# Kernel optimization log

Hardware: AMD Instinct MI355X
Metric: run time of the kernel (lower is better)

The kernel has to match this reference:

```python
import jax, jax.numpy as jnp
import numpy as np

TEMPERATURE = 0.07
EPS = 1e-8  # torch cosine_similarity norm clamp


def setup_inputs() -> dict:
    key = jax.random.key(0)
    k1, k2 = jax.random.split(key)
    B, d = 8192, 256
    X = jax.random.normal(k1, (B, d), dtype=jnp.float32)
    Y = jax.random.normal(k2, (B, d), dtype=jnp.float32)
    return {"X": X, "Y": Y}


def _normalize(v):
    # torch cosine_similarity clamps the norm at eps
    n = jnp.sqrt(jnp.sum(v * v, axis=-1, keepdims=True))
    return v / jnp.maximum(n, EPS)


def reference(X, Y):
    # cosine similarity matrix via normalize + GEMM (same math as broadcasted
    # cosine_similarity(X.unsqueeze(1), Y.unsqueeze(0), dim=-1))
    Xn = _normalize(X)                      # [B, d]
    Yn = _normalize(Y)                      # [B, d]
    logits = (Xn @ Yn.T) / TEMPERATURE      # [B, B]
    # cross_entropy with targets = arange(B): mean of -log_softmax diagonal
    logp = jax.nn.log_softmax(logits, axis=-1)
    loss = -jnp.mean(jnp.diagonal(logp))
    return loss
```

## Files before the change

kernel.cpp:

```cpp
#include <hip/hip_runtime.h>
#include <hip/hip_bf16.h>


typedef __attribute__((ext_vector_type(2)))  float f32x2;
typedef __attribute__((ext_vector_type(4)))  float f32x4;
typedef __attribute__((ext_vector_type(4)))  int   i32x4;
typedef __attribute__((ext_vector_type(8)))  int   i32x8;

#define AS1(p) ((const __attribute__((address_space(1))) void*)(uintptr_t)(p))
#define AS3(p) ((__attribute__((address_space(3))) void*)(uintptr_t)(p))

constexpr int   BROWS = 8192;
constexpr int   DDIM  = 256;
constexpr float kInvT = 14.285714285714286f;
constexpr float kC1   = 20.609929155556622f;
constexpr float kLn2  = 0.6931471805599453f;
constexpr int   kSC   = 0x7F7F7F7F;

#if __has_builtin(__builtin_amdgcn_exp2f)
#define EXP2F(x) __builtin_amdgcn_exp2f(x)
#else
#define EXP2F(x) exp2f(x)
#endif
#if __has_builtin(__builtin_amdgcn_logf)
#define LOG2F(x) __builtin_amdgcn_logf(x)
#else
#define LOG2F(x) log2f(x)
#endif

static __device__ __forceinline__ unsigned f2fp8(float f) {
  unsigned u = __builtin_bit_cast(unsigned, f);
  unsigned s = (u >> 24) & 0x80u;
  float af = __builtin_fabsf(f);
  if (af < 0.015625f) {
    int q = (int)__builtin_rintf(af * 512.0f);
    return s | (unsigned)q;
  }
  unsigned au = u & 0x7FFFFFFFu;
  au += 0x7FFFFu + ((au >> 20) & 1u);
  unsigned e8 = ((au >> 23) - 127u + 7u) & 0xFu;
  unsigned m  = (au >> 20) & 7u;
  return s | (e8 << 3) | m;
}

__global__ __launch_bounds__(256) void nrm_kernel(
    const float* __restrict__ X, const float* __restrict__ Y,
    unsigned int* __restrict__ Xq, unsigned int* __restrict__ Yq,
    float* __restrict__ diag, float* __restrict__ row_sum)
{
  const int wave = threadIdx.x >> 6;
  const int lane = threadIdx.x & 63;
  const int row  = blockIdx.x * 4 + wave;
  const float4 x = *(const float4*)(X + (size_t)row * DDIM + lane * 4);
  const float4 y = *(const float4*)(Y + (size_t)row * DDIM + lane * 4);
  float ssx = x.x*x.x + x.y*x.y + x.z*x.z + x.w*x.w;
  float ssy = y.x*y.x + y.y*y.y + y.z*y.z + y.w*y.w;
  float dot = x.x*y.x + x.y*y.y + x.z*y.z + x.w*y.w;
  #pragma unroll
  for (int m = 1; m < 64; m <<= 1) {
    ssx += __shfl_xor(ssx, m);
    ssy += __shfl_xor(ssy, m);
    dot += __shfl_xor(dot, m);
  }
  const float invx = 1.0f / fmaxf(sqrtf(ssx), 1e-8f);
  const float invy = 1.0f / fmaxf(sqrtf(ssy), 1e-8f);
#if __has_builtin(__builtin_amdgcn_cvt_pk_fp8_f32)
  int xq = __builtin_amdgcn_cvt_pk_fp8_f32(x.x * invx, x.y * invx, 0, false);
  xq     = __builtin_amdgcn_cvt_pk_fp8_f32(x.z * invx, x.w * invx, xq, true);
  int yq = __builtin_amdgcn_cvt_pk_fp8_f32(y.x * invy, y.y * invy, 0, false);
  yq     = __builtin_amdgcn_cvt_pk_fp8_f32(y.z * invy, y.w * invy, yq, true);
#else
  int xq = (int)(f2fp8(x.x*invx) | (f2fp8(x.y*invx) << 8) |
                 (f2fp8(x.z*invx) << 16) | (f2fp8(x.w*invx) << 24));
  int yq = (int)(f2fp8(y.x*invy) | (f2fp8(y.y*invy) << 8) |
                 (f2fp8(y.z*invy) << 16) | (f2fp8(y.w*invy) << 24));
#endif
  Xq[row * 64 + lane] = (unsigned)xq;
  Yq[row * 64 + lane] = (unsigned)yq;
  if (lane == 0) {
    diag[row] = dot * invx * invy * kInvT;
    row_sum[row] = 0.0f;
  }
}

static __device__ __forceinline__ void expflush(f32x4 (&pm)[2], f32x2 (&sm)[2]) {
  #pragma unroll
  for (int n = 0; n < 2; ++n) {
    f32x2 v0 = { pm[n][0], pm[n][1] };
    f32x2 v1 = { pm[n][2], pm[n][3] };
    v0 = v0 * kC1 + (f32x2){-kC1, -kC1};
    v1 = v1 * kC1 + (f32x2){-kC1, -kC1};
    sm[0] += (f32x2){ EXP2F(v0.x), EXP2F(v0.y) };
    sm[1] += (f32x2){ EXP2F(v1.x), EXP2F(v1.y) };
  }
}

static __device__ __forceinline__ void tile_step(
    const char* __restrict__ tb, const int (&bb)[2], const i32x8 (&a)[4][2],
    f32x4 (&cur)[4][2], f32x4 (&prev)[4][2], f32x2 (&sums2)[4][2])
{
  i32x8 b[2];
  __builtin_amdgcn_s_setprio(1);
  #pragma unroll
  for (int n = 0; n < 2; ++n) {
    const i32x4 lo = *(const i32x4*)(tb + (bb[n]));
    const i32x4 hi = *(const i32x4*)(tb + (bb[n] ^ 16));
    b[n] = __builtin_shufflevector(lo, hi, 0, 1, 2, 3, 4, 5, 6, 7);
  }
  #pragma unroll
  for (int m = 0; m < 4; ++m) {
    cur[m][0] = __builtin_amdgcn_mfma_scale_f32_16x16x128_f8f6f4(
        a[m][0], b[0], (f32x4){0.f, 0.f, 0.f, 0.f}, 0, 0, 0, kSC, 0, kSC);
    cur[m][1] = __builtin_amdgcn_mfma_scale_f32_16x16x128_f8f6f4(
        a[m][0], b[1], (f32x4){0.f, 0.f, 0.f, 0.f}, 0, 0, 0, kSC, 0, kSC);
  }
  __builtin_amdgcn_s_setprio(0);
  expflush(prev[0], sums2[0]);
  expflush(prev[1], sums2[1]);
  __builtin_amdgcn_s_setprio(1);
  #pragma unroll
  for (int n = 0; n < 2; ++n) {
    const i32x4 lo = *(const i32x4*)(tb + (bb[n] ^ 128));
    const i32x4 hi = *(const i32x4*)(tb + (bb[n] ^ 144));
    b[n] = __builtin_shufflevector(lo, hi, 0, 1, 2, 3, 4, 5, 6, 7);
  }
  #pragma unroll
  for (int m = 0; m < 4; ++m) {
    cur[m][0] = __builtin_amdgcn_mfma_scale_f32_16x16x128_f8f6f4(
        a[m][1], b[0], cur[m][0], 0, 0, 0, kSC, 0, kSC);
    cur[m][1] = __builtin_amdgcn_mfma_scale_f32_16x16x128_f8f6f4(
        a[m][1], b[1], cur[m][1], 0, 0, 0, kSC, 0, kSC);
  }
  __builtin_amdgcn_s_setprio(0);
  expflush(prev[2], sums2[2]);
  expflush(prev[3], sums2[3]);
}

__global__ __launch_bounds__(256, 2) void logits_kernel(
    const unsigned char* __restrict__ Xq,
    const unsigned char* __restrict__ Yq,
    float* __restrict__ row_sum)
{
  __shared__ char lds[4 * 8192];
  const int tid  = threadIdx.x;
  const int lane = tid & 63;
  const int wave = tid >> 6;
  const int l15  = lane & 15;
  const int g    = lane >> 4;

  const int bid  = blockIdx.x;
  const int xcd  = bid & 7;
  const int idx  = bid >> 3;
  const int panel = (xcd >> 2) * 16 + (idx & 15);
  const int split = (xcd & 3) * 4 + (idx >> 4);

  const int rowbase = panel * 256 + wave * 64;
  const char* Xb = (const char*)Xq;
  const char* Yb = (const char*)Yq + (size_t)split * (512 * 256);

  i32x8 a[4][2];
  #pragma unroll
  for (int m = 0; m < 4; ++m) {
    const char* rp = Xb + (size_t)(rowbase + m * 16 + l15) * 256 + g * 32;
    a[m][0] = *(const i32x8*)(rp);
    a[m][1] = *(const i32x8*)(rp + 128);
  }

  f32x2 sums2[4][2];
  #pragma unroll
  for (int m = 0; m < 4; ++m) {
    sums2[m][0] = (f32x2){0.f, 0.f};
    sums2[m][1] = (f32x2){0.f, 0.f};
  }

  int bb[2];
  #pragma unroll
  for (int n = 0; n < 2; ++n)
    bb[n] = (n * 16 + l15) * 256 + (((2 * g) ^ l15) << 4);

  auto stage = [&](int t, int buf) {
    const char* Yt = Yb + (size_t)t * 8192;
    char* db = lds + buf * 8192;
    #pragma unroll
    for (int s = 0; s < 2; ++s) {
      const int portion = (s * 4 + wave) * 1024;
      const int L = portion + lane * 16;
      const int src = (L & ~255) | ((L & 255) ^ (((L >> 8) & 15) << 4));
      __builtin_amdgcn_global_load_lds(AS1(Yt + src), AS3(db + portion), 16, 0, 0);
    }
  };

  f32x4 accA[4][2], accB[4][2];
  #pragma unroll
  for (int m = 0; m < 4; ++m)
    #pragma unroll
    for (int n = 0; n < 2; ++n) {
      accA[m][n] = (f32x4){0.f, 0.f, 0.f, 0.f};
      const float ni = -__builtin_inff();
      accB[m][n] = (f32x4){ni, ni, ni, ni};
    }

  stage(0, 0);
  stage(1, 1);
  stage(2, 2);
  #pragma unroll 1
  for (int p = 0; p < 8; ++p) {
    const int t = 2 * p;
    if (p < 7) asm volatile("s_waitcnt vmcnt(4)" ::: "memory");
    else       asm volatile("s_waitcnt vmcnt(2)" ::: "memory");
    __builtin_amdgcn_s_barrier();
    if (t + 3 < 16) stage(t + 3, (t + 3) & 3);
    tile_step(lds + (t & 3) * 8192, bb, a, accA, accB, sums2);
    if (p < 7) asm volatile("s_waitcnt vmcnt(4)" ::: "memory");
    else       asm volatile("s_waitcnt vmcnt(0)" ::: "memory");
    __builtin_amdgcn_s_barrier();
    if (t + 4 < 16) stage(t + 4, (t + 4) & 3);
    tile_step(lds + ((t + 1) & 3) * 8192, bb, a, accB, accA, sums2);
  }
  #pragma unroll
  for (int m = 0; m < 4; ++m)
    expflush(accB[m], sums2[m]);

  #pragma unroll
  for (int m = 0; m < 4; ++m)
    #pragma unroll
    for (int h = 0; h < 2; ++h)
      #pragma unroll
      for (int r2 = 0; r2 < 2; ++r2) {
        float s = (r2 == 0) ? sums2[m][h].x : sums2[m][h].y;
        s += __shfl_xor(s, 1);
        s += __shfl_xor(s, 2);
        s += __shfl_xor(s, 4);
        s += __shfl_xor(s, 8);
        if (l15 == 0)
          atomicAdd(row_sum + rowbase + m * 16 + g * 4 + h * 2 + r2, s);
      }
}

__global__ __launch_bounds__(1024) void loss_kernel(
    const float* __restrict__ row_sum, const float* __restrict__ diag,
    float* __restrict__ out)
{
  const int t = threadIdx.x;
  double acc = 0.0;
  #pragma unroll
  for (int h = 0; h < 2; ++h) {
    const int i = h * 4096 + t * 4;
    const float4 s = *(const float4*)(row_sum + i);
    const float4 d = *(const float4*)(diag + i);
    acc += (double)(kInvT + LOG2F(s.x) * kLn2 - d.x);
    acc += (double)(kInvT + LOG2F(s.y) * kLn2 - d.y);
    acc += (double)(kInvT + LOG2F(s.z) * kLn2 - d.z);
    acc += (double)(kInvT + LOG2F(s.w) * kLn2 - d.w);
  }
  #pragma unroll
  for (int m = 1; m < 64; m <<= 1) acc += __shfl_xor(acc, m);
  __shared__ double red[16];
  if ((t & 63) == 0) red[t >> 6] = acc;
  __syncthreads();
  if (t == 0) {
    double tot = 0.0;
    #pragma unroll
    for (int w = 0; w < 16; ++w) tot += red[w];
    out[0] = (float)(tot / (double)BROWS);
  }
}

extern "C" void kernel_launch(void* const* d_in, const int* in_sizes, int n_in,
                              void* d_out, int out_size, void* d_ws, size_t ws_size,
                              hipStream_t stream) {
  (void)in_sizes; (void)n_in; (void)out_size; (void)ws_size;
  const float* X = (const float*)d_in[0];
  const float* Y = (const float*)d_in[1];
  char* w = (char*)d_ws;
  unsigned int* Xq = (unsigned int*)(w);
  unsigned int* Yq = (unsigned int*)(w + (2u << 20));
  float* diag    = (float*)(w + (4u << 20));
  float* row_sum = (float*)(w + (4u << 20) + (32u << 10));

  nrm_kernel<<<BROWS / 4, 256, 0, stream>>>(X, Y, Xq, Yq, diag, row_sum);
  logits_kernel<<<512, 256, 0, stream>>>((const unsigned char*)Xq,
                                         (const unsigned char*)Yq, row_sum);
  loss_kernel<<<1, 1024, 0, stream>>>(row_sum, diag, (float*)d_out);
}
```

Baseline: 34.77 us.

## Fuse loss reduction into logits kernel and interleave exp with MFMA scheduling

Removes the separate loss kernel launch. A global atomic counter lets the last logits block do the final log-sum and mean. Inside tile_step, the exp work on the previous tile is interleaved one-by-one with the MFMAs, and sched_group_barrier hints replace the setprio blocks, aiming to overlap the transcendental work with matrix ops. This adds a threadfence and an atomic per block, plus a serial tail on one block.

```diff
diff --git a/kernel.cpp b/kernel.cpp
--- a/kernel.cpp
+++ b/kernel.cpp
@@ -9,6 +9,7 @@
 
 #define AS1(p) ((const __attribute__((address_space(1))) void*)(uintptr_t)(p))
 #define AS3(p) ((__attribute__((address_space(3))) void*)(uintptr_t)(p))
+#define SGB    __builtin_amdgcn_sched_group_barrier
 
 constexpr int   BROWS = 8192;
 constexpr int   DDIM  = 256;
@@ -46,7 +47,8 @@
 __global__ __launch_bounds__(256) void nrm_kernel(
     const float* __restrict__ X, const float* __restrict__ Y,
     unsigned int* __restrict__ Xq, unsigned int* __restrict__ Yq,
-    float* __restrict__ diag, float* __restrict__ row_sum)
+    float* __restrict__ diag, float* __restrict__ row_sum,
+    int* __restrict__ counter)
 {
   const int wave = threadIdx.x >> 6;
   const int lane = threadIdx.x & 63;
@@ -81,67 +83,86 @@
     diag[row] = dot * invx * invy * kInvT;
     row_sum[row] = 0.0f;
   }
-}
-
-static __device__ __forceinline__ void expflush(f32x4 (&pm)[2], f32x2 (&sm)[2]) {
-  #pragma unroll
-  for (int n = 0; n < 2; ++n) {
-    f32x2 v0 = { pm[n][0], pm[n][1] };
-    f32x2 v1 = { pm[n][2], pm[n][3] };
-    v0 = v0 * kC1 + (f32x2){-kC1, -kC1};
-    v1 = v1 * kC1 + (f32x2){-kC1, -kC1};
-    sm[0] += (f32x2){ EXP2F(v0.x), EXP2F(v0.y) };
-    sm[1] += (f32x2){ EXP2F(v1.x), EXP2F(v1.y) };
-  }
+  if (blockIdx.x == 0 && threadIdx.x == 0) counter[0] = 0;
+}
+
+static __device__ __forceinline__ void expq(const f32x4& pv, f32x2 (&sm)[2]) {
+  f32x2 v0 = { pv[0], pv[1] };
+  f32x2 v1 = { pv[2], pv[3] };
+  v0 = v0 * kC1 + (f32x2){-kC1, -kC1};
+  v1 = v1 * kC1 + (f32x2){-kC1, -kC1};
+  sm[0] += (f32x2){ EXP2F(v0.x), EXP2F(v0.y) };
+  sm[1] += (f32x2){ EXP2F(v1.x), EXP2F(v1.y) };
 }
 
 static __device__ __forceinline__ void tile_step(
     const char* __restrict__ tb, const int (&bb)[2], const i32x8 (&a)[4][2],
     f32x4 (&cur)[4][2], f32x4 (&prev)[4][2], f32x2 (&sums2)[4][2])
 {
-  i32x8 b[2];
-  __builtin_amdgcn_s_setprio(1);
-  #pragma unroll
-  for (int n = 0; n < 2; ++n) {
-    const i32x4 lo = *(const i32x4*)(tb + (bb[n]));
-    const i32x4 hi = *(const i32x4*)(tb + (bb[n] ^ 16));
-    b[n] = __builtin_shufflevector(lo, hi, 0, 1, 2, 3, 4, 5, 6, 7);
-  }
-  #pragma unroll
-  for (int m = 0; m < 4; ++m) {
-    cur[m][0] = __builtin_amdgcn_mfma_scale_f32_16x16x128_f8f6f4(
-        a[m][0], b[0], (f32x4){0.f, 0.f, 0.f, 0.f}, 0, 0, 0, kSC, 0, kSC);
-    cur[m][1] = __builtin_amdgcn_mfma_scale_f32_16x16x128_f8f6f4(
-        a[m][0], b[1], (f32x4){0.f, 0.f, 0.f, 0.f}, 0, 0, 0, kSC, 0, kSC);
-  }
-  __builtin_amdgcn_s_setprio(0);
-  expflush(prev[0], sums2[0]);
-  expflush(prev[1], sums2[1]);
-  __builtin_amdgcn_s_setprio(1);
-  #pragma unroll
-  for (int n = 0; n < 2; ++n) {
-    const i32x4 lo = *(const i32x4*)(tb + (bb[n] ^ 128));
-    const i32x4 hi = *(const i32x4*)(tb + (bb[n] ^ 144));
-    b[n] = __builtin_shufflevector(lo, hi, 0, 1, 2, 3, 4, 5, 6, 7);
-  }
-  #pragma unroll
-  for (int m = 0; m < 4; ++m) {
-    cur[m][0] = __builtin_amdgcn_mfma_scale_f32_16x16x128_f8f6f4(
-        a[m][1], b[0], cur[m][0], 0, 0, 0, kSC, 0, kSC);
-    cur[m][1] = __builtin_amdgcn_mfma_scale_f32_16x16x128_f8f6f4(
-        a[m][1], b[1], cur[m][1], 0, 0, 0, kSC, 0, kSC);
-  }
-  __builtin_amdgcn_s_setprio(0);
-  expflush(prev[2], sums2[2]);
-  expflush(prev[3], sums2[3]);
+  const f32x4 cz = {0.f, 0.f, 0.f, 0.f};
+  {
+    const i32x4 lo0 = *(const i32x4*)(tb + bb[0]);
+    const i32x4 hi0 = *(const i32x4*)(tb + (bb[0] ^ 16));
+    const i32x4 lo1 = *(const i32x4*)(tb + bb[1]);
+    const i32x4 hi1 = *(const i32x4*)(tb + (bb[1] ^ 16));
+    const i32x8 b0 = __builtin_shufflevector(lo0, hi0, 0, 1, 2, 3, 4, 5, 6, 7);
+    const i32x8 b1 = __builtin_shufflevector(lo1, hi1, 0, 1, 2, 3, 4, 5, 6, 7);
+    expq(prev[0][0], sums2[0]);
+    cur[0][0] = __builtin_amdgcn_mfma_scale_f32_16x16x128_f8f6f4(a[0][0], b0, cz, 0, 0, 0, kSC, 0, kSC);
+    cur[0][1] = __builtin_amdgcn_mfma_scale_f32_16x16x128_f8f6f4(a[0][0], b1, cz, 0, 0, 0, kSC, 0, kSC);
+    expq(prev[0][1], sums2[0]);
+    cur[1][0] = __builtin_amdgcn_mfma_scale_f32_16x16x128_f8f6f4(a[1][0], b0, cz, 0, 0, 0, kSC, 0, kSC);
+    cur[1][1] = __builtin_amdgcn_mfma_scale_f32_16x16x128_f8f6f4(a[1][0], b1, cz, 0, 0, 0, kSC, 0, kSC);
+    expq(prev[1][0], sums2[1]);
+    cur[2][0] = __builtin_amdgcn_mfma_scale_f32_16x16x128_f8f6f4(a[2][0], b0, cz, 0, 0, 0, kSC, 0, kSC);
+    cur[2][1] = __builtin_amdgcn_mfma_scale_f32_16x16x128_f8f6f4(a[2][0], b1, cz, 0, 0, 0, kSC, 0, kSC);
+    expq(prev[1][1], sums2[1]);
+    cur[3][0] = __builtin_amdgcn_mfma_scale_f32_16x16x128_f8f6f4(a[3][0], b0, cz, 0, 0, 0, kSC, 0, kSC);
+    cur[3][1] = __builtin_amdgcn_mfma_scale_f32_16x16x128_f8f6f4(a[3][0], b1, cz, 0, 0, 0, kSC, 0, kSC);
+    SGB(0x100, 4, 0);
+    SGB(0x002, 8, 0); SGB(0x008, 2, 0);
+    SGB(0x002, 8, 0); SGB(0x008, 2, 0);
+    SGB(0x002, 8, 0); SGB(0x008, 2, 0);
+    SGB(0x002, 8, 0); SGB(0x008, 2, 0);
+  }
+  {
+    const i32x4 lo0 = *(const i32x4*)(tb + (bb[0] ^ 128));
+    const i32x4 hi0 = *(const i32x4*)(tb + (bb[0] ^ 144));
+    const i32x4 lo1 = *(const i32x4*)(tb + (bb[1] ^ 128));
+    const i32x4 hi1 = *(const i32x4*)(tb + (bb[1] ^ 144));
+    const i32x8 b0 = __builtin_shufflevector(lo0, hi0, 0, 1, 2, 3, 4, 5, 6, 7);
+    const i32x8 b1 = __builtin_shufflevector(lo1, hi1, 0, 1, 2, 3, 4, 5, 6, 7);
+    expq(prev[2][0], sums2[2]);
+    cur[0][0] = __builtin_amdgcn_mfma_scale_f32_16x16x128_f8f6f4(a[0][1], b0, cur[0][0], 0, 0, 0, kSC, 0, kSC);
+    cur[0][1] = __builtin_amdgcn_mfma_scale_f32_16x16x128_f8f6f4(a[0][1], b1, cur[0][1], 0, 0, 0, kSC, 0, kSC);
+    expq(prev[2][1], sums2[2]);
+    cur[1][0] = __builtin_amdgcn_mfma_scale_f32_16x16x128_f8f6f4(a[1][1], b0, cur[1][0], 0, 0, 0, kSC, 0, kSC);
+    cur[1][1] = __builtin_amdgcn_mfma_scale_f32_16x16x128_f8f6f4(a[1][1], b1, cur[1][1], 0, 0, 0, kSC, 0, kSC);
+    expq(prev[3][0], sums2[3]);
+    cur[2][0] = __builtin_amdgcn_mfma_scale_f32_16x16x128_f8f6f4(a[2][1], b0, cur[2][0], 0, 0, 0, kSC, 0, kSC);
+    cur[2][1] = __builtin_amdgcn_mfma_scale_f32_16x16x128_f8f6f4(a[2][1], b1, cur[2][1], 0, 0, 0, kSC, 0, kSC);
+    expq(prev[3][1], sums2[3]);
+    cur[3][0] = __builtin_amdgcn_mfma_scale_f32_16x16x128_f8f6f4(a[3][1], b0, cur[3][0], 0, 0, 0, kSC, 0, kSC);
+    cur[3][1] = __builtin_amdgcn_mfma_scale_f32_16x16x128_f8f6f4(a[3][1], b1, cur[3][1], 0, 0, 0, kSC, 0, kSC);
+    SGB(0x100, 4, 0);
+    SGB(0x002, 8, 0); SGB(0x008, 2, 0);
+    SGB(0x002, 8, 0); SGB(0x008, 2, 0);
+    SGB(0x002, 8, 0); SGB(0x008, 2, 0);
+    SGB(0x002, 8, 0); SGB(0x008, 2, 0);
+  }
 }
 
 __global__ __launch_bounds__(256, 2) void logits_kernel(
     const unsigned char* __restrict__ Xq,
     const unsigned char* __restrict__ Yq,
-    float* __restrict__ row_sum)
+    float* __restrict__ row_sum,
+    const float* __restrict__ diag,
+    int* __restrict__ counter,
+    float* __restrict__ out)
 {
   __shared__ char lds[4 * 8192];
+  __shared__ int lastBlk;
+  __shared__ double red[4];
   const int tid  = threadIdx.x;
   const int lane = tid & 63;
   const int wave = tid >> 6;
@@ -218,8 +239,10 @@
     tile_step(lds + ((t + 1) & 3) * 8192, bb, a, accB, accA, sums2);
   }
   #pragma unroll
-  for (int m = 0; m < 4; ++m)
-    expflush(accB[m], sums2[m]);
+  for (int m = 0; m < 4; ++m) {
+    expq(accB[m][0], sums2[m]);
+    expq(accB[m][1], sums2[m]);
+  }
 
   #pragma unroll
   for (int m = 0; m < 4; ++m)
@@ -235,34 +258,32 @@
         if (l15 == 0)
           atomicAdd(row_sum + rowbase + m * 16 + g * 4 + h * 2 + r2, s);
       }
-}
-
-__global__ __launch_bounds__(1024) void loss_kernel(
-    const float* __restrict__ row_sum, const float* __restrict__ diag,
-    float* __restrict__ out)
-{
-  const int t = threadIdx.x;
-  double acc = 0.0;
-  #pragma unroll
-  for (int h = 0; h < 2; ++h) {
-    const int i = h * 4096 + t * 4;
-    const float4 s = *(const float4*)(row_sum + i);
-    const float4 d = *(const float4*)(diag + i);
-    acc += (double)(kInvT + LOG2F(s.x) * kLn2 - d.x);
-    acc += (double)(kInvT + LOG2F(s.y) * kLn2 - d.y);
-    acc += (double)(kInvT + LOG2F(s.z) * kLn2 - d.z);
-    acc += (double)(kInvT + LOG2F(s.w) * kLn2 - d.w);
-  }
-  #pragma unroll
-  for (int m = 1; m < 64; m <<= 1) acc += __shfl_xor(acc, m);
-  __shared__ double red[16];
-  if ((t & 63) == 0) red[t >> 6] = acc;
+
+  __threadfence();
+  if (tid == 0) {
+    const int old = atomicAdd(counter, 1);
+    lastBlk = (old == 511);
+  }
   __syncthreads();
-  if (t == 0) {
-    double tot = 0.0;
-    #pragma unroll
-    for (int w = 0; w < 16; ++w) tot += red[w];
-    out[0] = (float)(tot / (double)BROWS);
+  if (lastBlk) {
+    __threadfence();
+    double acc = 0.0;
+    #pragma unroll
+    for (int h2 = 0; h2 < 8; ++h2) {
+      const int i = h2 * 1024 + tid * 4;
+      const float4 s = *(const float4*)(row_sum + i);
+      const float4 d = *(const float4*)(diag + i);
+      acc += (double)(kInvT + LOG2F(s.x) * kLn2 - d.x);
+      acc += (double)(kInvT + LOG2F(s.y) * kLn2 - d.y);
+      acc += (double)(kInvT + LOG2F(s.z) * kLn2 - d.z);
+      acc += (double)(kInvT + LOG2F(s.w) * kLn2 - d.w);
+    }
+    #pragma unroll
+    for (int m = 1; m < 64; m <<= 1) acc += __shfl_xor(acc, m);
+    if (lane == 0) red[wave] = acc;
+    __syncthreads();
+    if (tid == 0)
+      out[0] = (float)((red[0] + red[1] + red[2] + red[3]) / (double)BROWS);
   }
 }
 
@@ -277,9 +298,10 @@
   unsigned int* Yq = (unsigned int*)(w + (2u << 20));
   float* diag    = (float*)(w + (4u << 20));
   float* row_sum = (float*)(w + (4u << 20) + (32u << 10));
-
-  nrm_kernel<<<BROWS / 4, 256, 0, stream>>>(X, Y, Xq, Yq, diag, row_sum);
+  int*   counter = (int*)(w + (4u << 20) + (64u << 10));
+
+  nrm_kernel<<<BROWS / 4, 256, 0, stream>>>(X, Y, Xq, Yq, diag, row_sum, counter);
   logits_kernel<<<512, 256, 0, stream>>>((const unsigned char*)Xq,
-                                         (const unsigned char*)Yq, row_sum);
-  loss_kernel<<<1, 1024, 0, stream>>>(row_sum, diag, (float*)d_out);
-}
+                                         (const unsigned char*)Yq, row_sum,
+                                         diag, counter, (float*)d_out);
+}
```

Result: slower. 59.13 us (+70.1%).
